# Kernel optimization log

Measured on AMD Instinct MI355X. Metric: run time of the kernel, lower is better.

Reference implementation:

```python
import jax, jax.numpy as jnp
import numpy as np

N_NODES = 100000
N_EDGES = 1600000
D_IN = 128
D_OUT = 128


def setup_inputs() -> dict:
    key = jax.random.key(0)
    k1, k2, k3, k4, k5, k6 = jax.random.split(key, 6)
    x = jax.random.normal(k1, (N_NODES, D_IN), dtype=jnp.float32)
    adj_rows = jnp.sort(jax.random.randint(k2, (N_EDGES,), 0, N_NODES, dtype=jnp.int32))
    adj_cols = jax.random.randint(k3, (N_EDGES,), 0, N_NODES, dtype=jnp.int32)
    adj_vals = jax.random.uniform(k4, (N_EDGES,), dtype=jnp.float32)
    weight = jax.random.normal(k5, (D_OUT, D_IN), dtype=jnp.float32) * (1.0 / np.sqrt(D_IN))
    bias = jax.random.normal(k6, (D_OUT,), dtype=jnp.float32) * 0.01
    return {"x": x, "adj_rows": adj_rows, "adj_cols": adj_cols,
            "adj_vals": adj_vals, "weight": weight, "bias": bias}


def reference(x, adj_rows, adj_cols, adj_vals, weight, bias):
    # w_input = inputs @ W.T  -> [N, D_OUT]
    w_input = x @ weight.T
    # SpMM: out[r] = sum_e adj_vals[e] * w_input[cols[e]] for edges with rows[e] == r
    msgs = adj_vals[:, None] * w_input[adj_cols]          # [E, D_OUT]
    agg = jax.ops.segment_sum(msgs, adj_rows, num_segments=N_NODES)
    out = jax.nn.relu(agg + bias)
    return out.astype(jnp.float32)
```

## Files before the change

kernel.cpp:

```cpp
#include <hip/hip_runtime.h>
#include <hip/hip_bf16.h>

#define D 128
#define RPW 2

typedef __attribute__((ext_vector_type(8))) short bf16x8;
typedef __attribute__((ext_vector_type(4))) float f32x4;

__device__ __forceinline__ unsigned short f2bf(float f) {
    union { float f; unsigned u; } uf{f};
    unsigned r = uf.u + 0x7fffu + ((uf.u >> 16) & 1u);
    return (unsigned short)(r >> 16);
}
__device__ __forceinline__ unsigned packcv(float a, float b) {
    __hip_bfloat162 h = __float22bfloat162_rn(make_float2(a, b));
    union { __hip_bfloat162 h; unsigned u; } c{h};
    return c.u;
}
__device__ __forceinline__ float bflo(unsigned u) {
    union { unsigned u; float f; } c{u << 16};
    return c.f;
}
__device__ __forceinline__ float bfhi(unsigned u) {
    union { unsigned u; float f; } c{u & 0xffff0000u};
    return c.f;
}
__device__ __forceinline__ int pc_col(unsigned u) { return (int)(u & 0x1FFFFu); }
__device__ __forceinline__ float pc_val(unsigned u) {
    union { unsigned u; float f; } c{(u >> 1) & 0xFFFF0000u};
    return c.f;
}

#define FMA8(A, vv, u) \
    A[0] = fmaf(vv, bflo(u.x), A[0]); A[1] = fmaf(vv, bfhi(u.x), A[1]); \
    A[2] = fmaf(vv, bflo(u.y), A[2]); A[3] = fmaf(vv, bfhi(u.y), A[3]); \
    A[4] = fmaf(vv, bflo(u.z), A[4]); A[5] = fmaf(vv, bfhi(u.z), A[5]); \
    A[6] = fmaf(vv, bflo(u.w), A[6]); A[7] = fmaf(vv, bfhi(u.w), A[7]);

__global__ __launch_bounds__(256) void build_rowptr(const int* __restrict__ rows,
                                                    const int* __restrict__ cols,
                                                    const float* __restrict__ vals,
                                                    const float* __restrict__ W,
                                                    unsigned short* __restrict__ wbf,
                                                    unsigned* __restrict__ pc,
                                                    int2* __restrict__ rowptr,
                                                    int e, int n) {
    int i = blockIdx.x * 256 + threadIdx.x;
    if (i < D * D) wbf[i] = f2bf(W[i]);
    if (i >= e) return;

    pc[i] = ((unsigned)f2bf(vals[i]) << 17) | (unsigned)cols[i];

    int r = rows[i];
    int prev = (i == 0) ? -1 : rows[i - 1];
    int next = (i == e - 1) ? n : rows[i + 1];
    if (prev != r) {
        rowptr[r].x = i;
        for (int q = prev + 1; q < r; ++q) rowptr[q] = make_int2(i, i);
    }
    if (next != r) {
        rowptr[r].y = i + 1;
        if (i == e - 1)
            for (int q = r + 1; q < n; ++q) rowptr[q] = make_int2(e, e);
    }
}

__global__ __launch_bounds__(256) void gemm_mfma(const float* __restrict__ x,
                                                 const unsigned short* __restrict__ wbf,
                                                 unsigned short* __restrict__ wi,
                                                 int nrows) {
    __shared__ __align__(16) unsigned short Ws[128 * 128];

    const int tid = threadIdx.x;
    const int lane = tid & 63;
    const int row0 = blockIdx.x * 128 + (tid >> 6) * 32;
    const int lrow = lane & 15;
    const int lk8 = (lane >> 4) * 8;

    float4 xf[2][4][2];
#pragma unroll
    for (int xb = 0; xb < 2; ++xb)
#pragma unroll
        for (int kb = 0; kb < 4; ++kb) {
            int gr = min(row0 + xb * 16 + lrow, nrows - 1);
            const float4* p = (const float4*)(x + (size_t)gr * D + kb * 32 + lk8);
            xf[xb][kb][0] = p[0];
            xf[xb][kb][1] = p[1];
        }

#pragma unroll
    for (int it = 0; it < 8; ++it) {
        int elem = it * 2048 + tid * 8;
        int r = elem >> 7, k = elem & 127;
        int idx = (r * 128 + k) ^ ((r & 7) << 3);
        *(uint4*)&Ws[idx] = *(const uint4*)(wbf + elem);
    }
    __syncthreads();

    bf16x8 xfrag[2][4];
#pragma unroll
    for (int xb = 0; xb < 2; ++xb)
#pragma unroll
        for (int kb = 0; kb < 4; ++kb) {
            float4 f0 = xf[xb][kb][0], f1 = xf[xb][kb][1];
            union { bf16x8 v; unsigned u[4]; } cv;
            cv.u[0] = packcv(f0.x, f0.y);
            cv.u[1] = packcv(f0.z, f0.w);
            cv.u[2] = packcv(f1.x, f1.y);
            cv.u[3] = packcv(f1.z, f1.w);
            xfrag[xb][kb] = cv.v;
        }

    f32x4 acc[2][8];
#pragma unroll
    for (int xb = 0; xb < 2; ++xb)
#pragma unroll
        for (int cb = 0; cb < 8; ++cb)
            acc[xb][cb] = (f32x4){0.f, 0.f, 0.f, 0.f};

#pragma unroll
    for (int cb = 0; cb < 8; ++cb) {
#pragma unroll
        for (int kb = 0; kb < 4; ++kb) {
            int wrow = cb * 16 + lrow;
            int idx = (wrow * 128 + kb * 32 + lk8) ^ ((wrow & 7) << 3);
            bf16x8 wfrag = *(const bf16x8*)&Ws[idx];
            acc[0][cb] = __builtin_amdgcn_mfma_f32_16x16x32_bf16(wfrag, xfrag[0][kb], acc[0][cb], 0, 0, 0);
            acc[1][cb] = __builtin_amdgcn_mfma_f32_16x16x32_bf16(wfrag, xfrag[1][kb], acc[1][cb], 0, 0, 0);
        }
    }

#pragma unroll
    for (int xb = 0; xb < 2; ++xb) {
        int g = row0 + xb * 16 + lrow;
        if (g < nrows) {
#pragma unroll
            for (int cb = 0; cb < 8; ++cb) {
                uint2 o;
                o.x = packcv(acc[xb][cb][0], acc[xb][cb][1]);
                o.y = packcv(acc[xb][cb][2], acc[xb][cb][3]);
                *(uint2*)(wi + (size_t)g * D + cb * 16 + (lane >> 4) * 4) = o;
            }
        }
    }
}

__global__ __launch_bounds__(256) void spmm_relu(const unsigned short* __restrict__ wi,
                                                 const int2* __restrict__ rowptr,
                                                 const unsigned* __restrict__ pc,
                                                 const float* __restrict__ bias,
                                                 float* __restrict__ out,
                                                 int n) {
    const int lane = threadIdx.x & 63;
    const int R0 = (blockIdx.x * 4 + (threadIdx.x >> 6)) * RPW;
    if (R0 >= n) return;
    const int nr = min(RPW, n - R0);

    const int2 rp = rowptr[R0 + min(lane, nr - 1)];
    const int ch = (lane & 15) * 8;
    const int sub = lane >> 4;

    float4 b0 = *(const float4*)(bias + (lane & 15) * 8);
    float4 b1 = *(const float4*)(bias + (lane & 15) * 8 + 4);

    int st = __shfl(rp.x, 0), en = __shfl(rp.y, 0);
    unsigned u = 0;
    { int idx = st + lane; if (idx < en) u = pc[idx]; }

    for (int j = 0; j < nr; ++j) {
        int st_n = 0, en_n = 0; unsigned u_n = 0;
        if (j + 1 < nr) {
            st_n = __shfl(rp.x, j + 1); en_n = __shfl(rp.y, j + 1);
            int idx = st_n + lane; if (idx < en_n) u_n = pc[idx];
        }

        float a0[8] = {0.f, 0.f, 0.f, 0.f, 0.f, 0.f, 0.f, 0.f};
        float a1[8] = {0.f, 0.f, 0.f, 0.f, 0.f, 0.f, 0.f, 0.f};

        const int cnt = min(en - st, 64);
        if (cnt > 0) {
            unsigned mA[4], mB[4];
#pragma unroll
            for (int p = 0; p < 4; ++p) {
                mA[p] = __shfl(u, sub + 4 * p);
                mB[p] = __shfl(u, 16 + sub + 4 * p);
            }
            uint4 uA[4], uB[4];
#pragma unroll
            for (int p = 0; p < 4; ++p) uA[p] = *(const uint4*)(wi + (size_t)pc_col(mA[p]) * D + ch);
#pragma unroll
            for (int p = 0; p < 4; ++p) uB[p] = *(const uint4*)(wi + (size_t)pc_col(mB[p]) * D + ch);
#pragma unroll
            for (int p = 0; p < 4; ++p) {
                FMA8(a0, pc_val(mA[p]), uA[p]);
                FMA8(a1, pc_val(mB[p]), uB[p]);
            }
            for (int E = 32; E < cnt; E += 16) {
#pragma unroll
                for (int p = 0; p < 4; ++p) {
                    unsigned m = __shfl(u, E + sub + 4 * p);
                    uint4 uq = *(const uint4*)(wi + (size_t)pc_col(m) * D + ch);
                    FMA8(a0, pc_val(m), uq);
                }
            }
        }
        for (int base = st + 64; base < en; base += 64) {
            unsigned uu = 0;
            { int idx = base + lane; if (idx < en) uu = pc[idx]; }
            const int cnt2 = min(en - base, 64);
            for (int E = 0; E < cnt2; E += 16) {
#pragma unroll
                for (int p = 0; p < 4; ++p) {
                    unsigned m = __shfl(uu, E + sub + 4 * p);
                    uint4 uq = *(const uint4*)(wi + (size_t)pc_col(m) * D + ch);
                    FMA8(a1, pc_val(m), uq);
                }
            }
        }

        float r8[8];
#pragma unroll
        for (int t = 0; t < 8; ++t) {
            float s = a0[t] + a1[t];
            s += __shfl_xor(s, 16);
            s += __shfl_xor(s, 32);
            r8[t] = s;
        }
        if (lane < 16) {
            float4 o0, o1;
            o0.x = fmaxf(r8[0] + b0.x, 0.f);
            o0.y = fmaxf(r8[1] + b0.y, 0.f);
            o0.z = fmaxf(r8[2] + b0.z, 0.f);
            o0.w = fmaxf(r8[3] + b0.w, 0.f);
            o1.x = fmaxf(r8[4] + b1.x, 0.f);
            o1.y = fmaxf(r8[5] + b1.y, 0.f);
            o1.z = fmaxf(r8[6] + b1.z, 0.f);
            o1.w = fmaxf(r8[7] + b1.w, 0.f);
            *(float4*)(out + (size_t)(R0 + j) * D + lane * 8) = o0;
            *(float4*)(out + (size_t)(R0 + j) * D + lane * 8 + 4) = o1;
        }

        st = st_n; en = en_n; u = u_n;
    }
}

extern "C" void kernel_launch(void* const* d_in, const int* in_sizes, int n_in,
                              void* d_out, int out_size, void* d_ws, size_t ws_size,
                              hipStream_t stream) {
    const float* x        = (const float*)d_in[0];
    const int*   adj_rows = (const int*)d_in[1];
    const int*   adj_cols = (const int*)d_in[2];
    const float* adj_vals = (const float*)d_in[3];
    const float* weight   = (const float*)d_in[4];
    const float* bias     = (const float*)d_in[5];
    float*       out      = (float*)d_out;

    const int n = in_sizes[0] / D;
    const int e = in_sizes[1];

    unsigned short* wi = (unsigned short*)d_ws;
    size_t off = ((size_t)n * D * sizeof(unsigned short) + 255) & ~(size_t)255;
    int2* rowptr = (int2*)((char*)d_ws + off);
    unsigned* pc = (unsigned*)(rowptr + n);
    unsigned short* wbf = (unsigned short*)(pc + e);

    build_rowptr<<<(e + 255) / 256, 256, 0, stream>>>(adj_rows, adj_cols, adj_vals,
                                                      weight, wbf, pc, rowptr, e, n);

    gemm_mfma<<<(n + 127) / 128, 256, 0, stream>>>(x, wbf, wi, n);

    spmm_relu<<<(n + 4 * RPW - 1) / (4 * RPW), 256, 0, stream>>>(
        wi, rowptr, pc, bias, out, n);
}
```

Baseline: 94.31 us.

## Stage X tile into LDS via global_load_lds DMA, read W directly from global

```diff
diff --git a/kernel.cpp b/kernel.cpp
--- a/kernel.cpp
+++ b/kernel.cpp
@@ -29,6 +29,12 @@
 __device__ __forceinline__ float pc_val(unsigned u) {
     union { unsigned u; float f; } c{(u >> 1) & 0xFFFF0000u};
     return c.f;
+}
+
+__device__ __forceinline__ void lds_dma16(const float* g, float* l) {
+    __builtin_amdgcn_global_load_lds(
+        (const __attribute__((address_space(1))) unsigned*)g,
+        (__attribute__((address_space(3))) unsigned*)l, 16, 0, 0);
 }
 
 #define FMA8(A, vv, u) \
@@ -69,40 +75,39 @@
                                                  const unsigned short* __restrict__ wbf,
                                                  unsigned short* __restrict__ wi,
                                                  int nrows) {
-    __shared__ __align__(16) unsigned short Ws[128 * 128];
+    __shared__ __align__(16) float Xs[128 * 128];
 
     const int tid = threadIdx.x;
     const int lane = tid & 63;
-    const int row0 = blockIdx.x * 128 + (tid >> 6) * 32;
+    const int wv = tid >> 6;
+    const int row0 = blockIdx.x * 128;
+
+#pragma unroll
+    for (int it = 0; it < 16; ++it) {
+        int A = it * 4096 + wv * 1024 + lane * 16;
+        int row = A >> 9;
+        int inner = (A & 511) ^ ((row & 7) << 4);
+        int gr = min(row0 + row, nrows - 1);
+        const float* gsrc = x + (size_t)gr * D + (inner >> 2);
+        lds_dma16(gsrc, Xs + (it * 4096 + wv * 1024) / 4);
+    }
+    __syncthreads();
+
+    const int m_base = wv * 32;
     const int lrow = lane & 15;
     const int lk8 = (lane >> 4) * 8;
 
-    float4 xf[2][4][2];
+    bf16x8 xfrag[2][4];
 #pragma unroll
     for (int xb = 0; xb < 2; ++xb)
 #pragma unroll
         for (int kb = 0; kb < 4; ++kb) {
-            int gr = min(row0 + xb * 16 + lrow, nrows - 1);
-            const float4* p = (const float4*)(x + (size_t)gr * D + kb * 32 + lk8);
-            xf[xb][kb][0] = p[0];
-            xf[xb][kb][1] = p[1];
-        }
-
-#pragma unroll
-    for (int it = 0; it < 8; ++it) {
-        int elem = it * 2048 + tid * 8;
-        int r = elem >> 7, k = elem & 127;
-        int idx = (r * 128 + k) ^ ((r & 7) << 3);
-        *(uint4*)&Ws[idx] = *(const uint4*)(wbf + elem);
-    }
-    __syncthreads();
-
-    bf16x8 xfrag[2][4];
-#pragma unroll
-    for (int xb = 0; xb < 2; ++xb)
-#pragma unroll
-        for (int kb = 0; kb < 4; ++kb) {
-            float4 f0 = xf[xb][kb][0], f1 = xf[xb][kb][1];
+            int r = m_base + xb * 16 + lrow;
+            int innerB = (kb * 32 + lk8) * 4;
+            int b0 = r * 512 + ((innerB) ^ ((r & 7) << 4));
+            int b1 = r * 512 + ((innerB + 16) ^ ((r & 7) << 4));
+            f32x4 f0 = *(const f32x4*)((const char*)Xs + b0);
+            f32x4 f1 = *(const f32x4*)((const char*)Xs + b1);
             union { bf16x8 v; unsigned u[4]; } cv;
             cv.u[0] = packcv(f0.x, f0.y);
             cv.u[1] = packcv(f0.z, f0.w);
@@ -122,9 +127,7 @@
     for (int cb = 0; cb < 8; ++cb) {
 #pragma unroll
         for (int kb = 0; kb < 4; ++kb) {
-            int wrow = cb * 16 + lrow;
-            int idx = (wrow * 128 + kb * 32 + lk8) ^ ((wrow & 7) << 3);
-            bf16x8 wfrag = *(const bf16x8*)&Ws[idx];
+            bf16x8 wfrag = *(const bf16x8*)(wbf + (cb * 16 + lrow) * 128 + kb * 32 + lk8);
             acc[0][cb] = __builtin_amdgcn_mfma_f32_16x16x32_bf16(wfrag, xfrag[0][kb], acc[0][cb], 0, 0, 0);
             acc[1][cb] = __builtin_amdgcn_mfma_f32_16x16x32_bf16(wfrag, xfrag[1][kb], acc[1][cb], 0, 0, 0);
         }
@@ -132,7 +135,7 @@
 
 #pragma unroll
     for (int xb = 0; xb < 2; ++xb) {
-        int g = row0 + xb * 16 + lrow;
+        int g = row0 + m_base + xb * 16 + lrow;
         if (g < nrows) {
 #pragma unroll
             for (int cb = 0; cb < 8; ++cb) {
```

After: 104.0 us. +10.3%, slower.
